# Kernel optimization log

Measured on AMD Instinct MI355X. Metric: run time of the kernel, lower is better.

## Reference

```python
import jax, jax.numpy as jnp
import numpy as np

B, S, D, H = 64, 2048, 64, 128  # batch, seq_len, input_dim, rnn_hidden_dim


def setup_inputs() -> dict:
    key = jax.random.key(0)
    k = jax.random.split(key, 6)
    x = jax.random.normal(k[0], (B, S, D), dtype=jnp.float32)
    # LSTM params, keras gate order: i, f, g(candidate), o
    Wx = jax.random.normal(k[1], (D, 4 * H), dtype=jnp.float32) / np.sqrt(D)
    Wh = jax.random.normal(k[2], (H, 4 * H), dtype=jnp.float32) / np.sqrt(H)
    b = jnp.zeros((4 * H,), dtype=jnp.float32).at[H:2 * H].set(1.0)  # unit_forget_bias
    # Dense(1, sigmoid) head
    Wd = jax.random.normal(k[3], (H, 1), dtype=jnp.float32) / np.sqrt(H)
    bd = jnp.zeros((1,), dtype=jnp.float32)
    return {"x": x, "Wx": Wx, "Wh": Wh, "b": b, "Wd": Wd, "bd": bd}


def _lstm_seq(x, Wx, Wh, b):
    H_ = Wh.shape[0]
    # precompute input projections for all timesteps: [B,S,4H]
    xz = jnp.einsum('bsd,dg->bsg', x, Wx) + b

    def step(carry, xz_t):
        h, c = carry
        z = xz_t + h @ Wh  # [B,4H]
        i = jax.nn.sigmoid(z[:, :H_])
        f = jax.nn.sigmoid(z[:, H_:2 * H_])
        g = jnp.tanh(z[:, 2 * H_:3 * H_])
        o = jax.nn.sigmoid(z[:, 3 * H_:])
        c = f * c + i * g
        h = o * jnp.tanh(c)
        return (h, c), h

    h0 = jnp.zeros((x.shape[0], H_), dtype=x.dtype)
    c0 = jnp.zeros((x.shape[0], H_), dtype=x.dtype)
    _, hs = jax.lax.scan(step, (h0, c0), jnp.swapaxes(xz, 0, 1))  # hs: [S,B,H]
    return jnp.swapaxes(hs, 0, 1)  # [B,S,H]


def reference(x, Wx, Wh, b, Wd, bd):
    h = _lstm_seq(x, Wx, Wh, b)                 # [B,S,H]
    return jax.nn.sigmoid(h @ Wd + bd)          # [B,S,1]
```

## Files before the change

### kernel.cpp

```cpp
#include <hip/hip_runtime.h>

#define B_ 64
#define S_ 2048
#define D_ 64
#define H_ 128
#define G_ 512
#define CH 16

typedef float f32x4 __attribute__((ext_vector_type(4)));
typedef short bf16x8 __attribute__((ext_vector_type(8)));

#define MFMA16(a, b, c) __builtin_amdgcn_mfma_f32_16x16x32_bf16((a), (b), (c), 0, 0, 0)

__device__ __forceinline__ short f2bf(float f) {
    unsigned u = __builtin_bit_cast(unsigned, f);
    return (short)((u + 0x7FFFu + ((u >> 16) & 1u)) >> 16);
}
__device__ __forceinline__ float bflo(unsigned u) { return __builtin_bit_cast(float, u << 16); }
__device__ __forceinline__ float bfhi(unsigned u) { return __builtin_bit_cast(float, u & 0xFFFF0000u); }
__device__ __forceinline__ float sigm_f(float x) { return __builtin_amdgcn_rcpf(1.0f + __expf(-x)); }
__device__ __forceinline__ float tanh_f(float x) {
    return __builtin_amdgcn_rcpf(1.0f + __expf(-2.0f * x)) * 2.0f - 1.0f;
}

__launch_bounds__(512, 2)
__global__ void lstm_fused(const float* __restrict__ x, const float* __restrict__ Wx,
                           const float* __restrict__ Wh, const float* __restrict__ bias,
                           const float* __restrict__ Wd, const float* __restrict__ bd,
                           float* __restrict__ out) {
    const int tid = threadIdx.x;
    const int lane = tid & 63;
    const int wid = tid >> 6;
    const int l15 = lane & 15;
    const int l4 = lane >> 4;
    const int bb = blockIdx.x;

    __shared__ alignas(16) short hist[CH][H_];
    __shared__ alignas(16) short xbf[CH][72];
    __shared__ float xzc[CH][G_];

    ((unsigned*)hist)[tid] = 0u;
    ((unsigned*)hist)[tid + 512] = 0u;

    const int col0 = wid * 16 + l15;

    bf16x8 bh[4][4];
#pragma unroll
    for (int ct = 0; ct < 4; ++ct) {
        const int col = ct * H_ + col0;
#pragma unroll
        for (int kt = 0; kt < 4; ++kt) {
            bf16x8 v;
#pragma unroll
            for (int e = 0; e < 8; ++e)
                v[e] = f2bf(Wh[(kt * 32 + l4 * 8 + e) * G_ + col]);
            bh[ct][kt] = v;
        }
    }
    bf16x8 bx[4][2];
#pragma unroll
    for (int ct = 0; ct < 4; ++ct) {
        const int col = ct * H_ + col0;
#pragma unroll
        for (int kt = 0; kt < 2; ++kt) {
            bf16x8 v;
#pragma unroll
            for (int e = 0; e < 8; ++e)
                v[e] = f2bf(Wx[(kt * 32 + l4 * 8 + e) * G_ + col]);
            bx[ct][kt] = v;
        }
    }

    float bvr[4];
#pragma unroll
    for (int ct = 0; ct < 4; ++ct) bvr[ct] = bias[ct * H_ + col0];
    const float wd0 = Wd[lane * 2 + 0];
    const float wd1 = Wd[lane * 2 + 1];
    const float bdv = bd[0];
    float c_reg = 0.0f;

    const float* xb = x + (size_t)bb * S_ * D_;
    float* ob = out + (size_t)bb * S_;

    float xp0 = xb[tid * 2 + 0];
    float xp1 = xb[tid * 2 + 1];

    for (int t = 0; t < S_; ++t) {
        const int tm = t & (CH - 1);
        if (tm == 0) {
            xbf[tid >> 5][(tid & 31) * 2 + 0] = f2bf(xp0);
            xbf[tid >> 5][(tid & 31) * 2 + 1] = f2bf(xp1);
            __syncthreads();
            if (t + CH < S_) {
                xp0 = xb[(t + CH) * D_ + tid * 2 + 0];
                xp1 = xb[(t + CH) * D_ + tid * 2 + 1];
            }
#pragma unroll
            for (int ct = 0; ct < 4; ++ct) {
                f32x4 acc = {bvr[ct], bvr[ct], bvr[ct], bvr[ct]};
#pragma unroll
                for (int kt = 0; kt < 2; ++kt) {
                    const bf16x8 a = *reinterpret_cast<const bf16x8*>(
                        &xbf[l15][kt * 32 + l4 * 8]);
                    acc = MFMA16(a, bx[ct][kt], acc);
                }
                const int col = ct * H_ + col0;
#pragma unroll
                for (int r = 0; r < 4; ++r)
                    xzc[l4 * 4 + r][col] = acc[r];
            }
            if (t > 0) {
#pragma unroll
                for (int s = 0; s < 2; ++s) {
                    const int row = wid * 2 + s;
                    const unsigned hp = *reinterpret_cast<const unsigned*>(&hist[row][lane * 2]);
                    float p = bflo(hp) * wd0 + bfhi(hp) * wd1;
                    p += __shfl_xor(p, 1);  p += __shfl_xor(p, 2);  p += __shfl_xor(p, 4);
                    p += __shfl_xor(p, 8);  p += __shfl_xor(p, 16); p += __shfl_xor(p, 32);
                    if (lane == 0) ob[t - CH + row] = sigm_f(p + bdv);
                }
            }
            __syncthreads();
        }

        const short* hsrc = hist[(t + CH - 1) & (CH - 1)];
        const bf16x8 a0 = *reinterpret_cast<const bf16x8*>(&hsrc[ 0 + l4 * 8]);
        const bf16x8 a1 = *reinterpret_cast<const bf16x8*>(&hsrc[32 + l4 * 8]);
        const bf16x8 a2 = *reinterpret_cast<const bf16x8*>(&hsrc[64 + l4 * 8]);
        const bf16x8 a3 = *reinterpret_cast<const bf16x8*>(&hsrc[96 + l4 * 8]);
        const float xzi = xzc[tm][0 * H_ + col0];
        const float xzf = xzc[tm][1 * H_ + col0];
        const float xzg = xzc[tm][2 * H_ + col0];
        const float xzo = xzc[tm][3 * H_ + col0];

        const f32x4 zz = {0.f, 0.f, 0.f, 0.f};
        f32x4 p0a = zz, p0b = zz, p1a = zz, p1b = zz, p2a = zz, p2b = zz, p3a = zz, p3b = zz;
        p0a = MFMA16(a0, bh[0][0], p0a);  p0b = MFMA16(a2, bh[0][2], p0b);
        p1a = MFMA16(a0, bh[1][0], p1a);  p1b = MFMA16(a2, bh[1][2], p1b);
        p2a = MFMA16(a0, bh[2][0], p2a);  p2b = MFMA16(a2, bh[2][2], p2b);
        p3a = MFMA16(a0, bh[3][0], p3a);  p3b = MFMA16(a2, bh[3][2], p3b);
        p0a = MFMA16(a1, bh[0][1], p0a);  p0b = MFMA16(a3, bh[0][3], p0b);
        p1a = MFMA16(a1, bh[1][1], p1a);  p1b = MFMA16(a3, bh[1][3], p1b);
        p2a = MFMA16(a1, bh[2][1], p2a);  p2b = MFMA16(a3, bh[2][3], p2b);
        p3a = MFMA16(a1, bh[3][1], p3a);  p3b = MFMA16(a3, bh[3][3], p3b);

        const float zi = p0a[0] + p0b[0] + xzi;
        const float zf = p1a[0] + p1b[0] + xzf;
        const float zg = p2a[0] + p2b[0] + xzg;
        const float zo = p3a[0] + p3b[0] + xzo;

        const float ig = sigm_f(zi);
        const float fg = sigm_f(zf);
        const float og = sigm_f(zo);
        const float gg = tanh_f(zg);
        c_reg = fg * c_reg + ig * gg;
        const float hv = og * tanh_f(c_reg);

        if (lane < 16) hist[tm][col0] = f2bf(hv);
        __syncthreads();
    }

#pragma unroll
    for (int s = 0; s < 2; ++s) {
        const int row = wid * 2 + s;
        const unsigned hp = *reinterpret_cast<const unsigned*>(&hist[row][lane * 2]);
        float p = bflo(hp) * wd0 + bfhi(hp) * wd1;
        p += __shfl_xor(p, 1);  p += __shfl_xor(p, 2);  p += __shfl_xor(p, 4);
        p += __shfl_xor(p, 8);  p += __shfl_xor(p, 16); p += __shfl_xor(p, 32);
        if (lane == 0) ob[S_ - CH + row] = sigm_f(p + bdv);
    }
}

extern "C" void kernel_launch(void* const* d_in, const int* in_sizes, int n_in,
                              void* d_out, int out_size, void* d_ws, size_t ws_size,
                              hipStream_t stream) {
    const float* x  = (const float*)d_in[0];
    const float* Wx = (const float*)d_in[1];
    const float* Wh = (const float*)d_in[2];
    const float* b  = (const float*)d_in[3];
    const float* Wd = (const float*)d_in[4];
    const float* bd = (const float*)d_in[5];
    float* out = (float*)d_out;

    lstm_fused<<<B_, 512, 0, stream>>>(x, Wx, Wh, b, Wd, bd, out);
}
```

Measured before the change: 1.086 ms.

## Spread gate activations across lane groups and unroll timestep chunk loop

Measured after the change: 1.067 ms. Within noise of the previous version (-1.8%).

```diff
diff --git a/kernel.cpp b/kernel.cpp
--- a/kernel.cpp
+++ b/kernel.cpp
@@ -12,16 +12,22 @@
 
 #define MFMA16(a, b, c) __builtin_amdgcn_mfma_f32_16x16x32_bf16((a), (b), (c), 0, 0, 0)
 
+#if __has_builtin(__builtin_amdgcn_exp2f)
+#define EXP2(x) __builtin_amdgcn_exp2f(x)
+#else
+#define EXP2(x) exp2f(x)
+#endif
+#define RCPF(x) __builtin_amdgcn_rcpf(x)
+
+#define LOG2E 1.442695041f
+
 __device__ __forceinline__ short f2bf(float f) {
     unsigned u = __builtin_bit_cast(unsigned, f);
     return (short)((u + 0x7FFFu + ((u >> 16) & 1u)) >> 16);
 }
 __device__ __forceinline__ float bflo(unsigned u) { return __builtin_bit_cast(float, u << 16); }
 __device__ __forceinline__ float bfhi(unsigned u) { return __builtin_bit_cast(float, u & 0xFFFF0000u); }
-__device__ __forceinline__ float sigm_f(float x) { return __builtin_amdgcn_rcpf(1.0f + __expf(-x)); }
-__device__ __forceinline__ float tanh_f(float x) {
-    return __builtin_amdgcn_rcpf(1.0f + __expf(-2.0f * x)) * 2.0f - 1.0f;
-}
+__device__ __forceinline__ float sigm_f(float x) { return RCPF(1.0f + EXP2(x * -LOG2E)); }
 
 __launch_bounds__(512, 2)
 __global__ void lstm_fused(const float* __restrict__ x, const float* __restrict__ Wx,
@@ -43,6 +49,8 @@
     ((unsigned*)hist)[tid + 512] = 0u;
 
     const int col0 = wid * 16 + l15;
+    const bool b0 = (l4 & 1) != 0;
+    const bool b1 = (l4 & 2) != 0;
 
     bf16x8 bh[4][4];
 #pragma unroll
@@ -79,85 +87,100 @@
     const float bdv = bd[0];
     float c_reg = 0.0f;
 
+    const float m_c = (l4 == 2) ? (-2.0f * LOG2E) : (-LOG2E);
+    const float a_c = (l4 == 2) ? 2.0f : 1.0f;
+    const float b_c = (l4 == 2) ? -1.0f : 0.0f;
+
     const float* xb = x + (size_t)bb * S_ * D_;
     float* ob = out + (size_t)bb * S_;
 
     float xp0 = xb[tid * 2 + 0];
     float xp1 = xb[tid * 2 + 1];
 
-    for (int t = 0; t < S_; ++t) {
-        const int tm = t & (CH - 1);
-        if (tm == 0) {
-            xbf[tid >> 5][(tid & 31) * 2 + 0] = f2bf(xp0);
-            xbf[tid >> 5][(tid & 31) * 2 + 1] = f2bf(xp1);
+    for (int tc = 0; tc < S_; tc += CH) {
+        xbf[tid >> 5][(tid & 31) * 2 + 0] = f2bf(xp0);
+        xbf[tid >> 5][(tid & 31) * 2 + 1] = f2bf(xp1);
+        __syncthreads();
+        if (tc + CH < S_) {
+            xp0 = xb[(tc + CH) * D_ + tid * 2 + 0];
+            xp1 = xb[(tc + CH) * D_ + tid * 2 + 1];
+        }
+#pragma unroll
+        for (int ct = 0; ct < 4; ++ct) {
+            f32x4 acc = {bvr[ct], bvr[ct], bvr[ct], bvr[ct]};
+#pragma unroll
+            for (int kt = 0; kt < 2; ++kt) {
+                const bf16x8 a = *reinterpret_cast<const bf16x8*>(&xbf[l15][kt * 32 + l4 * 8]);
+                acc = MFMA16(a, bx[ct][kt], acc);
+            }
+#pragma unroll
+            for (int r = 0; r < 4; ++r)
+                xzc[l4 * 4 + r][col0 * 4 + ct] = acc[r];
+        }
+        if (tc > 0) {
+#pragma unroll
+            for (int s = 0; s < 2; ++s) {
+                const int row = wid * 2 + s;
+                const unsigned hp = *reinterpret_cast<const unsigned*>(&hist[row][lane * 2]);
+                float p = bflo(hp) * wd0 + bfhi(hp) * wd1;
+                p += __shfl_xor(p, 1);  p += __shfl_xor(p, 2);  p += __shfl_xor(p, 4);
+                p += __shfl_xor(p, 8);  p += __shfl_xor(p, 16); p += __shfl_xor(p, 32);
+                if (lane == 0) ob[tc - CH + row] = sigm_f(p + bdv);
+            }
+        }
+        __syncthreads();
+
+#pragma unroll
+        for (int tm = 0; tm < CH; ++tm) {
+            const int prev = (tm + CH - 1) & (CH - 1);
+            const short* hsrc = hist[prev];
+            const bf16x8 a0 = *reinterpret_cast<const bf16x8*>(&hsrc[ 0 + l4 * 8]);
+            const bf16x8 a1 = *reinterpret_cast<const bf16x8*>(&hsrc[32 + l4 * 8]);
+            const bf16x8 a2 = *reinterpret_cast<const bf16x8*>(&hsrc[64 + l4 * 8]);
+            const bf16x8 a3 = *reinterpret_cast<const bf16x8*>(&hsrc[96 + l4 * 8]);
+            const float xz1 = xzc[tm][col0 * 4 + l4];
+
+            const f32x4 zz = {0.f, 0.f, 0.f, 0.f};
+            f32x4 acc0 = zz, acc1 = zz, acc2 = zz, acc3 = zz;
+            acc0 = MFMA16(a0, bh[0][0], acc0);
+            acc1 = MFMA16(a0, bh[1][0], acc1);
+            acc2 = MFMA16(a0, bh[2][0], acc2);
+            acc3 = MFMA16(a0, bh[3][0], acc3);
+            acc0 = MFMA16(a1, bh[0][1], acc0);
+            acc1 = MFMA16(a1, bh[1][1], acc1);
+            acc2 = MFMA16(a1, bh[2][1], acc2);
+            acc3 = MFMA16(a1, bh[3][1], acc3);
+            acc0 = MFMA16(a2, bh[0][2], acc0);
+            acc1 = MFMA16(a2, bh[1][2], acc1);
+            acc2 = MFMA16(a2, bh[2][2], acc2);
+            acc3 = MFMA16(a2, bh[3][2], acc3);
+            acc0 = MFMA16(a3, bh[0][3], acc0);
+            acc1 = MFMA16(a3, bh[1][3], acc1);
+            acc2 = MFMA16(a3, bh[2][3], acc2);
+            acc3 = MFMA16(a3, bh[3][3], acc3);
+
+            float zsel = b1 ? (b0 ? acc3[0] : acc2[0]) : (b0 ? acc1[0] : acc0[0]);
+            zsel += xz1;
+
+            const float t = a_c * RCPF(1.0f + EXP2(zsel * m_c)) + b_c;
+
+            const float r1 = __shfl_xor(t, 16);
+            const float r2 = __shfl_xor(t, 32);
+            const float r3 = __shfl_xor(r2, 16);
+            const float iv = b1 ? (b0 ? r3 : r2) : (b0 ? r1 : t);
+            const float fv = b1 ? (b0 ? r2 : r3) : (b0 ? t  : r1);
+            const float gv = b1 ? (b0 ? r1 : t ) : (b0 ? r3 : r2);
+            const float ov = b1 ? (b0 ? t  : r1) : (b0 ? r2 : r3);
+
+            c_reg = fv * c_reg + iv * gv;
+            const float th = 2.0f * RCPF(1.0f + EXP2(c_reg * (-2.0f * LOG2E))) - 1.0f;
+            const float hv = ov * th;
+
+            unsigned hb;
+            asm("v_cvt_pk_bf16_f32 %0, %1, %2" : "=v"(hb) : "v"(hv), "v"(0.0f));
+            if (lane < 16) hist[tm][col0] = (short)hb;
             __syncthreads();
-            if (t + CH < S_) {
-                xp0 = xb[(t + CH) * D_ + tid * 2 + 0];
-                xp1 = xb[(t + CH) * D_ + tid * 2 + 1];
-            }
-#pragma unroll
-            for (int ct = 0; ct < 4; ++ct) {
-                f32x4 acc = {bvr[ct], bvr[ct], bvr[ct], bvr[ct]};
-#pragma unroll
-                for (int kt = 0; kt < 2; ++kt) {
-                    const bf16x8 a = *reinterpret_cast<const bf16x8*>(
-                        &xbf[l15][kt * 32 + l4 * 8]);
-                    acc = MFMA16(a, bx[ct][kt], acc);
-                }
-                const int col = ct * H_ + col0;
-#pragma unroll
-                for (int r = 0; r < 4; ++r)
-                    xzc[l4 * 4 + r][col] = acc[r];
-            }
-            if (t > 0) {
-#pragma unroll
-                for (int s = 0; s < 2; ++s) {
-                    const int row = wid * 2 + s;
-                    const unsigned hp = *reinterpret_cast<const unsigned*>(&hist[row][lane * 2]);
-                    float p = bflo(hp) * wd0 + bfhi(hp) * wd1;
-                    p += __shfl_xor(p, 1);  p += __shfl_xor(p, 2);  p += __shfl_xor(p, 4);
-                    p += __shfl_xor(p, 8);  p += __shfl_xor(p, 16); p += __shfl_xor(p, 32);
-                    if (lane == 0) ob[t - CH + row] = sigm_f(p + bdv);
-                }
-            }
-            __syncthreads();
-        }
-
-        const short* hsrc = hist[(t + CH - 1) & (CH - 1)];
-        const bf16x8 a0 = *reinterpret_cast<const bf16x8*>(&hsrc[ 0 + l4 * 8]);
-        const bf16x8 a1 = *reinterpret_cast<const bf16x8*>(&hsrc[32 + l4 * 8]);
-        const bf16x8 a2 = *reinterpret_cast<const bf16x8*>(&hsrc[64 + l4 * 8]);
-        const bf16x8 a3 = *reinterpret_cast<const bf16x8*>(&hsrc[96 + l4 * 8]);
-        const float xzi = xzc[tm][0 * H_ + col0];
-        const float xzf = xzc[tm][1 * H_ + col0];
-        const float xzg = xzc[tm][2 * H_ + col0];
-        const float xzo = xzc[tm][3 * H_ + col0];
-
-        const f32x4 zz = {0.f, 0.f, 0.f, 0.f};
-        f32x4 p0a = zz, p0b = zz, p1a = zz, p1b = zz, p2a = zz, p2b = zz, p3a = zz, p3b = zz;
-        p0a = MFMA16(a0, bh[0][0], p0a);  p0b = MFMA16(a2, bh[0][2], p0b);
-        p1a = MFMA16(a0, bh[1][0], p1a);  p1b = MFMA16(a2, bh[1][2], p1b);
-        p2a = MFMA16(a0, bh[2][0], p2a);  p2b = MFMA16(a2, bh[2][2], p2b);
-        p3a = MFMA16(a0, bh[3][0], p3a);  p3b = MFMA16(a2, bh[3][2], p3b);
-        p0a = MFMA16(a1, bh[0][1], p0a);  p0b = MFMA16(a3, bh[0][3], p0b);
-        p1a = MFMA16(a1, bh[1][1], p1a);  p1b = MFMA16(a3, bh[1][3], p1b);
-        p2a = MFMA16(a1, bh[2][1], p2a);  p2b = MFMA16(a3, bh[2][3], p2b);
-        p3a = MFMA16(a1, bh[3][1], p3a);  p3b = MFMA16(a3, bh[3][3], p3b);
-
-        const float zi = p0a[0] + p0b[0] + xzi;
-        const float zf = p1a[0] + p1b[0] + xzf;
-        const float zg = p2a[0] + p2b[0] + xzg;
-        const float zo = p3a[0] + p3b[0] + xzo;
-
-        const float ig = sigm_f(zi);
-        const float fg = sigm_f(zf);
-        const float og = sigm_f(zo);
-        const float gg = tanh_f(zg);
-        c_reg = fg * c_reg + ig * gg;
-        const float hv = og * tanh_f(c_reg);
-
-        if (lane < 16) hist[tm][col0] = f2bf(hv);
-        __syncthreads();
+        }
     }
 
 #pragma unroll
```
